# Performance work log

Hardware: AMD Instinct MI355X
Metric: run time of the kernel (lower is better)

## Reference

```python
import jax, jax.numpy as jnp
import numpy as np


def setup_inputs() -> dict:
    key = jax.random.key(0)
    ks = jax.random.split(key, 7)
    B, S, D, H = 8, 1024, 1024, 16
    dk = D // H
    return {
        "q": jax.random.normal(ks[0], (B, S, D), dtype=jnp.float32),
        "k": jax.random.normal(ks[1], (B, S, D), dtype=jnp.float32),
        "v": jax.random.normal(ks[2], (B, S, D), dtype=jnp.float32),
        "Wq": jax.random.normal(ks[3], (H, dk, D), dtype=jnp.float32) * 0.03,
        "Wk": jax.random.normal(ks[4], (H, dk, D), dtype=jnp.float32) * 0.03,
        "Wv": jax.random.normal(ks[5], (dk, D), dtype=jnp.float32) * 0.03,
        "Wo": jax.random.normal(ks[6], (D, dk), dtype=jnp.float32) * 0.03,
    }


def reference(q, k, v, Wq, Wk, Wv, Wo):
    # per-head projections (Linear weight layout [out, in]); shared V projection
    dk = Wq.shape[1]
    qs = jnp.einsum("bsd,hed->bhse", q, Wq)          # [B,H,S,dk]
    ks_ = jnp.einsum("btd,hed->bhte", k, Wk)         # [B,H,S,dk]
    vs = jnp.einsum("btd,ed->bte", v, Wv)            # [B,S,dk] shared across heads
    scale = jnp.sqrt(jnp.asarray(dk, dtype=qs.dtype))
    scores = jnp.einsum("bhse,bhte->bhst", qs, ks_) / scale
    attn = jax.nn.softmax(scores, axis=-1)           # [B,H,Sq,Sk]
    heads = jnp.einsum("bhst,bte->bhse", attn, vs)   # [B,H,S,dk]
    head_mean = jnp.mean(heads, axis=1)              # mean over heads -> [B,S,dk]
    outputs = jnp.einsum("bse,de->bsd", head_mean, Wo)
    attn_out = jnp.transpose(attn, (0, 2, 1, 3))     # stacked at dim=2: [B,Sq,H,Sk]
    return outputs, attn_out
```

## Files before the change

### kernel.cpp

```cpp
#include <hip/hip_runtime.h>
#include <hip/hip_bf16.h>


typedef __attribute__((ext_vector_type(4))) float f32x4;
typedef __attribute__((ext_vector_type(8))) short bf16x8;
typedef __attribute__((ext_vector_type(2))) unsigned int uint2v;

#define MFMA16(a, b, c) __builtin_amdgcn_mfma_f32_16x16x32_bf16((a), (b), (c), 0, 0, 0)

__device__ __forceinline__ unsigned int rne16(float f) {
  unsigned int u = __float_as_uint(f);
  return u + 0x7fffu + ((u >> 16) & 1u);
}
__device__ __forceinline__ unsigned int pack2bf(float a, float b) {
  return (rne16(a) >> 16) | (rne16(b) & 0xffff0000u);
}
__device__ __forceinline__ short f2bf(float f) {
  return (short)(rne16(f) >> 16);
}
__device__ __forceinline__ float bf2f(short s) {
  return __uint_as_float(((unsigned int)(unsigned short)s) << 16);
}
__device__ __forceinline__ float bflo(unsigned int u) {
  return __uint_as_float(u << 16);
}
__device__ __forceinline__ float bfhi(unsigned int u) {
  return __uint_as_float(u & 0xffff0000u);
}

__global__ __launch_bounds__(256) void proj_qk_kernel(
    const float* __restrict__ qin, const float* __restrict__ kin,
    const float* __restrict__ Wq, const float* __restrict__ Wk,
    __hip_bfloat16* __restrict__ qs, __hip_bfloat16* __restrict__ ks)
{
  const int K = 1024, N = 1024;
  __shared__ short a_lds[128][40];
  __shared__ short b_lds[128][40];
  const int tid  = threadIdx.x;
  const int lane = tid & 63, wid = tid >> 6;
  const int g = lane >> 4, r = lane & 15;
  const bool isK = blockIdx.y >= 8;
  const float* A = isK ? kin : qin;
  const float* W = isK ? Wk : Wq;
  __hip_bfloat16* C = isK ? ks : qs;
  const float scale = isK ? 1.0f : 0.125f;
  const int m0 = blockIdx.x * 128;
  const int n0 = (blockIdx.y & 7) * 128;
  const int wm = (wid >> 1) * 64, wn = (wid & 1) * 64;
  const int lrow = tid >> 3, lcol = (tid & 7) * 4;

  f32x4 acc[4][4];
#pragma unroll
  for (int i = 0; i < 4; ++i)
#pragma unroll
    for (int j = 0; j < 4; ++j) acc[i][j] = (f32x4){0.f, 0.f, 0.f, 0.f};

  for (int k0 = 0; k0 < K; k0 += 32) {
    float4 av[4], wv[4];
#pragma unroll
    for (int p = 0; p < 4; ++p) {
      av[p] = *(const float4*)&A[(m0 + lrow + p * 32) * K + k0 + lcol];
      wv[p] = *(const float4*)&W[(n0 + lrow + p * 32) * K + k0 + lcol];
    }
    __syncthreads();
#pragma unroll
    for (int p = 0; p < 4; ++p) {
      uint2v ua = {pack2bf(av[p].x, av[p].y), pack2bf(av[p].z, av[p].w)};
      uint2v uw = {pack2bf(wv[p].x, wv[p].y), pack2bf(wv[p].z, wv[p].w)};
      *(uint2v*)&a_lds[lrow + p * 32][lcol] = ua;
      *(uint2v*)&b_lds[lrow + p * 32][lcol] = uw;
    }
    __syncthreads();
    bf16x8 af[4], bf[4];
#pragma unroll
    for (int t = 0; t < 4; ++t) {
      af[t] = *(bf16x8*)&a_lds[wm + t * 16 + r][g * 8];
      bf[t] = *(bf16x8*)&b_lds[wn + t * 16 + r][g * 8];
    }
#pragma unroll
    for (int mt = 0; mt < 4; ++mt)
#pragma unroll
      for (int nt = 0; nt < 4; ++nt)
        acc[mt][nt] = MFMA16(af[mt], bf[nt], acc[mt][nt]);
  }

#pragma unroll
  for (int mt = 0; mt < 4; ++mt)
#pragma unroll
    for (int nt = 0; nt < 4; ++nt) {
      const int n = n0 + wn + nt * 16 + r;
#pragma unroll
      for (int j = 0; j < 4; ++j) {
        const int m = m0 + wm + mt * 16 + 4 * g + j;
        C[m * N + n] = __float2bfloat16(acc[mt][nt][j] * scale);
      }
    }
}

__global__ __launch_bounds__(256) void proj_v_kernel(
    const float* __restrict__ vin, const float* __restrict__ Wv,
    __hip_bfloat16* __restrict__ vsT)
{
  const int K = 1024;
  __shared__ short a_lds[128][40];
  __shared__ short b_lds[64][40];
  const int tid  = threadIdx.x;
  const int lane = tid & 63, wid = tid >> 6;
  const int g = lane >> 4, r = lane & 15;
  const int m0 = blockIdx.x * 128;
  const int wm = wid * 32;
  const int lrow = tid >> 3, lcol = (tid & 7) * 4;

  f32x4 acc[2][4];
#pragma unroll
  for (int i = 0; i < 2; ++i)
#pragma unroll
    for (int j = 0; j < 4; ++j) acc[i][j] = (f32x4){0.f, 0.f, 0.f, 0.f};

  for (int k0 = 0; k0 < K; k0 += 32) {
    float4 av[4], wv2[2];
#pragma unroll
    for (int p = 0; p < 4; ++p)
      av[p] = *(const float4*)&vin[(m0 + lrow + p * 32) * K + k0 + lcol];
#pragma unroll
    for (int p = 0; p < 2; ++p)
      wv2[p] = *(const float4*)&Wv[(lrow + p * 32) * K + k0 + lcol];
    __syncthreads();
#pragma unroll
    for (int p = 0; p < 4; ++p) {
      uint2v ua = {pack2bf(av[p].x, av[p].y), pack2bf(av[p].z, av[p].w)};
      *(uint2v*)&a_lds[lrow + p * 32][lcol] = ua;
    }
#pragma unroll
    for (int p = 0; p < 2; ++p) {
      uint2v uw = {pack2bf(wv2[p].x, wv2[p].y), pack2bf(wv2[p].z, wv2[p].w)};
      *(uint2v*)&b_lds[lrow + p * 32][lcol] = uw;
    }
    __syncthreads();
    bf16x8 af[2], bf[4];
#pragma unroll
    for (int t = 0; t < 2; ++t) af[t] = *(bf16x8*)&a_lds[wm + t * 16 + r][g * 8];
#pragma unroll
    for (int t = 0; t < 4; ++t) bf[t] = *(bf16x8*)&b_lds[t * 16 + r][g * 8];
#pragma unroll
    for (int mt = 0; mt < 2; ++mt)
#pragma unroll
      for (int nt = 0; nt < 4; ++nt)
        acc[mt][nt] = MFMA16(af[mt], bf[nt], acc[mt][nt]);
  }

#pragma unroll
  for (int mt = 0; mt < 2; ++mt)
#pragma unroll
    for (int nt = 0; nt < 4; ++nt) {
      const int e = nt * 16 + r;
#pragma unroll
      for (int j = 0; j < 4; ++j) {
        const int m = m0 + wm + mt * 16 + 4 * g + j;
        const int b = m >> 10, t = m & 1023;
        vsT[b * 65536 + e * 1024 + t] = __float2bfloat16(acc[mt][nt][j]);
      }
    }
}

__global__ __launch_bounds__(1024, 4) void attn_kernel(
    const __hip_bfloat16* __restrict__ qs_, const __hip_bfloat16* __restrict__ ks_,
    const __hip_bfloat16* __restrict__ vsT_, float* __restrict__ attn_out,
    __hip_bfloat16* __restrict__ heads_)
{
  const int S = 1024, H = 16;
  const int tid = threadIdx.x, lane = tid & 63, wid = tid >> 6;
  const int g = lane >> 4, r = lane & 15;
  const int qg = wid & 3, kc = wid >> 2;
  const int qb = blockIdx.x, h = blockIdx.y, b = blockIdx.z;
  const int bh = b * H + h;
  const int qrow = qb * 64 + qg * 16;

  __shared__ short p_lds[16][16][40];
  __shared__ float heads_lds[64][80];
  __shared__ float l_lds[4][4][16];

  const short* qsp = (const short*)qs_;
  const short* ksp = (const short*)ks_;
  const short* vsp = (const short*)vsT_;
  short* headsp = (short*)heads_;

  const int qidx = (b * S + qrow + r) * 1024 + h * 64;
  const bf16x8 qf0 = *(const bf16x8*)&qsp[qidx + g * 8];
  const bf16x8 qf1 = *(const bf16x8*)&qsp[qidx + 32 + g * 8];
  const int kbase = (b * S + kc * 256 + r) * 1024 + h * 64 + g * 8;

  unsigned int pk[32];
  float lsa0 = 0.f, lsa1 = 0.f, lsa2 = 0.f, lsa3 = 0.f;
#pragma unroll
  for (int i = 0; i < 4; ++i) {
    const int t0 = i * 64;
    bf16x8 kf[8];
#pragma unroll
    for (int u = 0; u < 4; ++u) {
      kf[2 * u]     = *(const bf16x8*)&ksp[kbase + (t0 + 16 * u) * 1024];
      kf[2 * u + 1] = *(const bf16x8*)&ksp[kbase + (t0 + 16 * u) * 1024 + 32];
    }
    float es[4];
#pragma unroll
    for (int u = 0; u < 4; ++u) {
      f32x4 s = (f32x4){0.f, 0.f, 0.f, 0.f};
      s = MFMA16(kf[2 * u], qf0, s);
      s = MFMA16(kf[2 * u + 1], qf1, s);
      const float e0 = __expf(s[0]), e1 = __expf(s[1]);
      const float e2 = __expf(s[2]), e3 = __expf(s[3]);
      pk[i * 8 + 2 * u]     = pack2bf(e0, e1);
      pk[i * 8 + 2 * u + 1] = pack2bf(e2, e3);
      es[u] = (e0 + e1) + (e2 + e3);
    }
    lsa0 += es[0]; lsa1 += es[1]; lsa2 += es[2]; lsa3 += es[3];
  }
  float ls = (lsa0 + lsa1) + (lsa2 + lsa3);
  ls += __shfl_xor(ls, 16);
  ls += __shfl_xor(ls, 32);
  if (g == 0) l_lds[kc][qg][r] = ls;
  __syncthreads();
  const float lf = (l_lds[0][qg][r] + l_lds[1][qg][r]) +
                   (l_lds[2][qg][r] + l_lds[3][qg][r]);
  const float inv = 1.f / lf;
  float invq[4];
#pragma unroll
  for (int j = 0; j < 4; ++j) invq[j] = __shfl(inv, 4 * g + j);

  f32x4 hacc[4];
#pragma unroll
  for (int i = 0; i < 4; ++i) hacc[i] = (f32x4){0.f, 0.f, 0.f, 0.f};

  const int arow = ((b * S + qrow + r) * H + h) * S + kc * 256;
  const int vbase = b * 65536 + r * 1024 + g * 8 + kc * 256;

#pragma unroll
  for (int j = 0; j < 8; ++j) {
    const int tcl = j * 32;
    bf16x8 vf[4];
#pragma unroll
    for (int nt = 0; nt < 4; ++nt)
      vf[nt] = *(const bf16x8*)&vsp[vbase + nt * 16384 + tcl];
    uint2v w0 = {pk[4 * j + 0], pk[4 * j + 1]};
    uint2v w1 = {pk[4 * j + 2], pk[4 * j + 3]};
    *(uint2v*)&p_lds[wid][r][0 * 16 + 4 * g] = w0;
    *(uint2v*)&p_lds[wid][r][1 * 16 + 4 * g] = w1;
    f32x4 p0, p1;
    p0[0] = bflo(pk[4 * j + 0]) * inv; p0[1] = bfhi(pk[4 * j + 0]) * inv;
    p0[2] = bflo(pk[4 * j + 1]) * inv; p0[3] = bfhi(pk[4 * j + 1]) * inv;
    p1[0] = bflo(pk[4 * j + 2]) * inv; p1[1] = bfhi(pk[4 * j + 2]) * inv;
    p1[2] = bflo(pk[4 * j + 3]) * inv; p1[3] = bfhi(pk[4 * j + 3]) * inv;
    __builtin_nontemporal_store(p0, (f32x4*)&attn_out[arow + tcl + 4 * g]);
    __builtin_nontemporal_store(p1, (f32x4*)&attn_out[arow + tcl + 16 + 4 * g]);
    asm volatile("s_waitcnt lgkmcnt(0)" ::: "memory");
    const bf16x8 pa = *(bf16x8*)&p_lds[wid][r][g * 8];
#pragma unroll
    for (int nt = 0; nt < 4; ++nt)
      hacc[nt] = MFMA16(pa, vf[nt], hacc[nt]);
  }

  const int hrow = qg * 16 + 4 * g;
#pragma unroll
  for (int kk = 0; kk < 3; ++kk) {
    if (kc == kk) {
#pragma unroll
      for (int nt = 0; nt < 4; ++nt)
#pragma unroll
        for (int j = 0; j < 4; ++j) {
          float* p = &heads_lds[hrow + j][nt * 16 + r];
          *p = (kk == 0) ? hacc[nt][j] : (*p + hacc[nt][j]);
        }
    }
    __syncthreads();
  }
  if (kc == 3) {
#pragma unroll
    for (int nt = 0; nt < 4; ++nt)
#pragma unroll
      for (int j = 0; j < 4; ++j) {
        const float hv = heads_lds[hrow + j][nt * 16 + r] + hacc[nt][j];
        headsp[(bh * S + qrow + 4 * g + j) * 64 + nt * 16 + r] =
            f2bf(hv * invq[j]);
      }
  }
}

__global__ __launch_bounds__(256) void out_kernel(
    const __hip_bfloat16* __restrict__ heads_, const float* __restrict__ Wo,
    float* __restrict__ out)
{
  __shared__ float hm[16][64];
  const int tid = threadIdx.x;
  const int m0 = blockIdx.x * 16;
  const short* headsp = (const short*)heads_;

  {
    const int row = tid >> 4, e4 = (tid & 15) * 4;
    const int m = m0 + row, b = m >> 10, s = m & 1023;
    float a0 = 0.f, a1 = 0.f, a2 = 0.f, a3 = 0.f;
    for (int hh = 0; hh < 16; ++hh) {
      typedef __attribute__((ext_vector_type(4))) short short4v;
      const short4v hv =
          *(const short4v*)&headsp[((b * 16 + hh) * 1024 + s) * 64 + e4];
      a0 += bf2f(hv[0]); a1 += bf2f(hv[1]); a2 += bf2f(hv[2]); a3 += bf2f(hv[3]);
    }
    const float sc = 1.f / 16.f;
    hm[row][e4 + 0] = a0 * sc; hm[row][e4 + 1] = a1 * sc;
    hm[row][e4 + 2] = a2 * sc; hm[row][e4 + 3] = a3 * sc;
  }
  __syncthreads();

  for (int c = 0; c < 4; ++c) {
    const int d = c * 256 + tid;
    float4 wo4[16];
#pragma unroll
    for (int i = 0; i < 16; ++i) wo4[i] = *(const float4*)&Wo[d * 64 + i * 4];
    for (int row = 0; row < 16; ++row) {
      float a = 0.f;
#pragma unroll
      for (int i = 0; i < 16; ++i) {
        const float4 h4 = *(const float4*)&hm[row][i * 4];
        a += h4.x * wo4[i].x + h4.y * wo4[i].y + h4.z * wo4[i].z + h4.w * wo4[i].w;
      }
      out[(m0 + row) * 1024 + d] = a;
    }
  }
}

extern "C" void kernel_launch(void* const* d_in, const int* in_sizes, int n_in,
                              void* d_out, int out_size, void* d_ws, size_t ws_size,
                              hipStream_t stream) {
  const float* q  = (const float*)d_in[0];
  const float* k  = (const float*)d_in[1];
  const float* v  = (const float*)d_in[2];
  const float* Wq = (const float*)d_in[3];
  const float* Wk = (const float*)d_in[4];
  const float* Wv = (const float*)d_in[5];
  const float* Wo = (const float*)d_in[6];

  float* out0 = (float*)d_out;
  float* attn = out0 + (size_t)8 * 1024 * 1024;

  char* ws = (char*)d_ws;
  __hip_bfloat16* qs    = (__hip_bfloat16*)(ws);
  __hip_bfloat16* ksbuf = (__hip_bfloat16*)(ws + (16u << 20));
  __hip_bfloat16* vsT   = (__hip_bfloat16*)(ws + (32u << 20));
  __hip_bfloat16* heads = (__hip_bfloat16*)(ws + (33u << 20));

  proj_qk_kernel<<<dim3(64, 16), dim3(256), 0, stream>>>(q, k, Wq, Wk, qs, ksbuf);
  proj_v_kernel<<<dim3(64), dim3(256), 0, stream>>>(v, Wv, vsT);
  attn_kernel<<<dim3(16, 16, 8), dim3(1024), 0, stream>>>(qs, ksbuf, vsT, attn, heads);
  out_kernel<<<dim3(512), dim3(256), 0, stream>>>(heads, Wo, out0);
}
```

Measured before the change: 437.0 us.

## Shrink attention blocks to 256 threads and stage P once before PV loop

Each attention block now covers 16 query rows with 4 waves (one per key chunk) instead of 64 rows with 16 waves, launched as a 4x larger grid. All bf16 probabilities are written to LDS once before the PV loop, which removes the per-iteration LDS write and wait from that loop. The serial three-step cross-wave heads reduction is replaced by one parallel reduction through LDS that reuses the P buffer. This aims to cut barrier stalls and expose more independent blocks, at the cost of a larger LDS footprint per wave and more block launches.

```diff
diff --git a/kernel.cpp b/kernel.cpp
--- a/kernel.cpp
+++ b/kernel.cpp
@@ -4,6 +4,7 @@
 
 typedef __attribute__((ext_vector_type(4))) float f32x4;
 typedef __attribute__((ext_vector_type(8))) short bf16x8;
+typedef __attribute__((ext_vector_type(4))) short short4v;
 typedef __attribute__((ext_vector_type(2))) unsigned int uint2v;
 
 #define MFMA16(a, b, c) __builtin_amdgcn_mfma_f32_16x16x32_bf16((a), (b), (c), 0, 0, 0)
@@ -163,22 +164,21 @@
     }
 }
 
-__global__ __launch_bounds__(1024, 4) void attn_kernel(
+__global__ __launch_bounds__(256, 4) void attn_kernel(
     const __hip_bfloat16* __restrict__ qs_, const __hip_bfloat16* __restrict__ ks_,
     const __hip_bfloat16* __restrict__ vsT_, float* __restrict__ attn_out,
     __hip_bfloat16* __restrict__ heads_)
 {
   const int S = 1024, H = 16;
-  const int tid = threadIdx.x, lane = tid & 63, wid = tid >> 6;
+  const int tid = threadIdx.x, lane = tid & 63, kc = tid >> 6;
   const int g = lane >> 4, r = lane & 15;
-  const int qg = wid & 3, kc = wid >> 2;
-  const int qb = blockIdx.x, h = blockIdx.y, b = blockIdx.z;
+  const int h = blockIdx.y, b = blockIdx.z;
   const int bh = b * H + h;
-  const int qrow = qb * 64 + qg * 16;
-
-  __shared__ short p_lds[16][16][40];
-  __shared__ float heads_lds[64][80];
-  __shared__ float l_lds[4][4][16];
+  const int qrow = blockIdx.x * 16;
+
+  __shared__ short p_big[4][16][260];
+  __shared__ float l_lds[4][16];
+  float (*heads_ov)[16][80] = (float (*)[16][80])p_big;
 
   const short* qsp = (const short*)qs_;
   const short* ksp = (const short*)ks_;
@@ -218,14 +218,19 @@
   float ls = (lsa0 + lsa1) + (lsa2 + lsa3);
   ls += __shfl_xor(ls, 16);
   ls += __shfl_xor(ls, 32);
-  if (g == 0) l_lds[kc][qg][r] = ls;
+  if (g == 0) l_lds[kc][r] = ls;
   __syncthreads();
-  const float lf = (l_lds[0][qg][r] + l_lds[1][qg][r]) +
-                   (l_lds[2][qg][r] + l_lds[3][qg][r]);
+  const float lf = (l_lds[0][r] + l_lds[1][r]) + (l_lds[2][r] + l_lds[3][r]);
   const float inv = 1.f / lf;
-  float invq[4];
-#pragma unroll
-  for (int j = 0; j < 4; ++j) invq[j] = __shfl(inv, 4 * g + j);
+
+#pragma unroll
+  for (int j = 0; j < 8; ++j) {
+    uint2v w0 = {pk[4 * j + 0], pk[4 * j + 1]};
+    uint2v w1 = {pk[4 * j + 2], pk[4 * j + 3]};
+    *(uint2v*)&p_big[kc][r][j * 32 + 4 * g] = w0;
+    *(uint2v*)&p_big[kc][r][j * 32 + 16 + 4 * g] = w1;
+  }
+  asm volatile("s_waitcnt lgkmcnt(0)" ::: "memory");
 
   f32x4 hacc[4];
 #pragma unroll
@@ -241,10 +246,10 @@
 #pragma unroll
     for (int nt = 0; nt < 4; ++nt)
       vf[nt] = *(const bf16x8*)&vsp[vbase + nt * 16384 + tcl];
-    uint2v w0 = {pk[4 * j + 0], pk[4 * j + 1]};
-    uint2v w1 = {pk[4 * j + 2], pk[4 * j + 3]};
-    *(uint2v*)&p_lds[wid][r][0 * 16 + 4 * g] = w0;
-    *(uint2v*)&p_lds[wid][r][1 * 16 + 4 * g] = w1;
+    const bf16x8 pa = *(bf16x8*)&p_big[kc][r][tcl + g * 8];
+#pragma unroll
+    for (int nt = 0; nt < 4; ++nt)
+      hacc[nt] = MFMA16(pa, vf[nt], hacc[nt]);
     f32x4 p0, p1;
     p0[0] = bflo(pk[4 * j + 0]) * inv; p0[1] = bfhi(pk[4 * j + 0]) * inv;
     p0[2] = bflo(pk[4 * j + 1]) * inv; p0[3] = bfhi(pk[4 * j + 1]) * inv;
@@ -252,36 +257,29 @@
     p1[2] = bflo(pk[4 * j + 3]) * inv; p1[3] = bfhi(pk[4 * j + 3]) * inv;
     __builtin_nontemporal_store(p0, (f32x4*)&attn_out[arow + tcl + 4 * g]);
     __builtin_nontemporal_store(p1, (f32x4*)&attn_out[arow + tcl + 16 + 4 * g]);
-    asm volatile("s_waitcnt lgkmcnt(0)" ::: "memory");
-    const bf16x8 pa = *(bf16x8*)&p_lds[wid][r][g * 8];
-#pragma unroll
-    for (int nt = 0; nt < 4; ++nt)
-      hacc[nt] = MFMA16(pa, vf[nt], hacc[nt]);
-  }
-
-  const int hrow = qg * 16 + 4 * g;
-#pragma unroll
-  for (int kk = 0; kk < 3; ++kk) {
-    if (kc == kk) {
-#pragma unroll
-      for (int nt = 0; nt < 4; ++nt)
-#pragma unroll
-        for (int j = 0; j < 4; ++j) {
-          float* p = &heads_lds[hrow + j][nt * 16 + r];
-          *p = (kk == 0) ? hacc[nt][j] : (*p + hacc[nt][j]);
-        }
-    }
-    __syncthreads();
-  }
-  if (kc == 3) {
-#pragma unroll
-    for (int nt = 0; nt < 4; ++nt)
-#pragma unroll
-      for (int j = 0; j < 4; ++j) {
-        const float hv = heads_lds[hrow + j][nt * 16 + r] + hacc[nt][j];
-        headsp[(bh * S + qrow + 4 * g + j) * 64 + nt * 16 + r] =
-            f2bf(hv * invq[j]);
-      }
+  }
+  __syncthreads();
+
+#pragma unroll
+  for (int nt = 0; nt < 4; ++nt)
+#pragma unroll
+    for (int j = 0; j < 4; ++j)
+      heads_ov[kc][4 * g + j][nt * 16 + r] = hacc[nt][j];
+  __syncthreads();
+
+  {
+    const int row = tid >> 4, c4 = (tid & 15) * 4;
+    const float lrow = (l_lds[0][row] + l_lds[1][row]) +
+                       (l_lds[2][row] + l_lds[3][row]);
+    const float invr = 1.f / lrow;
+    short4v hv;
+#pragma unroll
+    for (int i = 0; i < 4; ++i) {
+      const float s4 = (heads_ov[0][row][c4 + i] + heads_ov[1][row][c4 + i]) +
+                       (heads_ov[2][row][c4 + i] + heads_ov[3][row][c4 + i]);
+      hv[i] = f2bf(s4 * invr);
+    }
+    *(short4v*)&headsp[(bh * S + qrow + row) * 64 + c4] = hv;
   }
 }
 
@@ -299,7 +297,6 @@
     const int m = m0 + row, b = m >> 10, s = m & 1023;
     float a0 = 0.f, a1 = 0.f, a2 = 0.f, a3 = 0.f;
     for (int hh = 0; hh < 16; ++hh) {
-      typedef __attribute__((ext_vector_type(4))) short short4v;
       const short4v hv =
           *(const short4v*)&headsp[((b * 16 + hh) * 1024 + s) * 64 + e4];
       a0 += bf2f(hv[0]); a1 += bf2f(hv[1]); a2 += bf2f(hv[2]); a3 += bf2f(hv[3]);
@@ -349,6 +346,6 @@
 
   proj_qk_kernel<<<dim3(64, 16), dim3(256), 0, stream>>>(q, k, Wq, Wk, qs, ksbuf);
   proj_v_kernel<<<dim3(64), dim3(256), 0, stream>>>(v, Wv, vsT);
-  attn_kernel<<<dim3(16, 16, 8), dim3(1024), 0, stream>>>(qs, ksbuf, vsT, attn, heads);
+  attn_kernel<<<dim3(64, 16, 8), dim3(256), 0, stream>>>(qs, ksbuf, vsT, attn, heads);
   out_kernel<<<dim3(512), dim3(256), 0, stream>>>(heads, Wo, out0);
 }
```

Measured after the change: 420.1 us. 3.9% less time.
